# Kernel optimization log

Measured on AMD Instinct MI355X. Metric: run time of the kernel, lower is better.

## Reference

```python
import jax, jax.numpy as jnp
import numpy as np

B, S, E, H = 2, 2048, 1024, 16
HD = E // H


def setup_inputs() -> dict:
    key = jax.random.key(0)
    k1, k2, k3, k4 = jax.random.split(key, 4)
    x = jax.random.normal(k1, (B, S, E), dtype=jnp.float32)
    # nn.Linear(E, 3E, bias=False): weight shape (3E, E), y = x @ W.T
    w_qkv = jax.random.normal(k2, (3 * E, E), dtype=jnp.float32) * (E ** -0.5)
    w_proj = jax.random.normal(k3, (E, E), dtype=jnp.float32) * (E ** -0.5)
    b_proj = jax.random.normal(k4, (E,), dtype=jnp.float32) * 0.02
    return {"x": x, "w_qkv": w_qkv, "w_proj": w_proj, "b_proj": b_proj}


def reference(x, w_qkv, w_proj, b_proj):
    b, s, e = x.shape
    hd = e // H
    qkv = x @ w_qkv.T                                   # (B,S,3E)
    qkv = qkv.reshape(b, s, H, 3, hd)                   # matches view(B,S,H,3*hd).chunk(3,-1)
    q = jnp.transpose(qkv[..., 0, :], (0, 2, 1, 3))      # (B,H,S,hd)
    k = jnp.transpose(qkv[..., 1, :], (0, 2, 1, 3))
    v = jnp.transpose(qkv[..., 2, :], (0, 2, 1, 3))
    scale = hd ** -0.5
    scores = jnp.einsum('bhqd,bhkd->bhqk', q, k) * scale  # (B,H,S,S)
    causal = jnp.tril(jnp.ones((s, s), dtype=bool))
    scores = jnp.where(causal, scores, jnp.float32(-jnp.inf))
    probs = jax.nn.softmax(scores, axis=-1)
    out = jnp.einsum('bhqk,bhkd->bhqd', probs, v)        # (B,H,S,hd)
    out = jnp.transpose(out, (0, 2, 1, 3)).reshape(b, s, e)
    return out @ w_proj.T + b_proj
```

## Files before the change

### kernel.cpp

```cpp
#include <hip/hip_runtime.h>
#include <hip/hip_bf16.h>

#define B_    2
#define S_    2048
#define E_    1024
#define H_    16
#define HD_   64
#define M_    (B_ * S_)
#define QKVN  (3 * E_)

typedef __attribute__((ext_vector_type(8))) short  short8;
typedef __attribute__((ext_vector_type(4))) float  f32x4;

static __device__ __forceinline__ unsigned short f2bf(float f) {
  union { float f; unsigned int u; } c; c.f = f;
  unsigned int u = c.u;
  return (unsigned short)((u + 0x7fffu + ((u >> 16) & 1u)) >> 16);
}

static __device__ __forceinline__ void gload16(unsigned short* lds,
                                               const unsigned short* g) {
  __builtin_amdgcn_global_load_lds(
      (__attribute__((address_space(1))) void*)g,
      (__attribute__((address_space(3))) void*)lds, 16, 0, 0);
}

static __device__ __forceinline__ float dpp_max16(float x) {
  x = fmaxf(x, __int_as_float(__builtin_amdgcn_update_dpp(
          0, __float_as_int(x), 0xB1, 0xF, 0xF, true)));
  x = fmaxf(x, __int_as_float(__builtin_amdgcn_update_dpp(
          0, __float_as_int(x), 0x4E, 0xF, 0xF, true)));
  x = fmaxf(x, __int_as_float(__builtin_amdgcn_update_dpp(
          0, __float_as_int(x), 0x141, 0xF, 0xF, true)));
  x = fmaxf(x, __int_as_float(__builtin_amdgcn_update_dpp(
          0, __float_as_int(x), 0x140, 0xF, 0xF, true)));
  return x;
}
static __device__ __forceinline__ float dpp_sum16(float x) {
  x += __int_as_float(__builtin_amdgcn_update_dpp(
          0, __float_as_int(x), 0xB1, 0xF, 0xF, true));
  x += __int_as_float(__builtin_amdgcn_update_dpp(
          0, __float_as_int(x), 0x4E, 0xF, 0xF, true));
  x += __int_as_float(__builtin_amdgcn_update_dpp(
          0, __float_as_int(x), 0x141, 0xF, 0xF, true));
  x += __int_as_float(__builtin_amdgcn_update_dpp(
          0, __float_as_int(x), 0x140, 0xF, 0xF, true));
  return x;
}

__global__ __launch_bounds__(256) void cvt_f32_to_bf16(
    const float* __restrict__ in, unsigned short* __restrict__ out, int n4) {
  int i = blockIdx.x * 256 + threadIdx.x;
  if (i < n4) {
    float4 v = reinterpret_cast<const float4*>(in)[i];
    ushort4 r;
    r.x = f2bf(v.x); r.y = f2bf(v.y); r.z = f2bf(v.z); r.w = f2bf(v.w);
    reinterpret_cast<ushort4*>(out)[i] = r;
  }
}

template <int BF16_OUT>
__global__ __launch_bounds__(256) void gemm_bt(
    const unsigned short* __restrict__ A, const unsigned short* __restrict__ Bt,
    void* __restrict__ Cout, const float* __restrict__ bias,
    int M, int N, int K, int ldc) {
  __shared__ alignas(16) unsigned short lds_a[128 * 64];
  __shared__ alignas(16) unsigned short lds_b[128 * 64];
  const int t  = threadIdx.x;
  const int w  = t >> 6, l = t & 63, g = l >> 4, lr = l & 15;
  const int bm = blockIdx.y * 128, bn = blockIdx.x * 128;
  const int wr = (w >> 1) * 64,  wc = (w & 1) * 64;

  f32x4 acc[4][4] = {};

  for (int k0 = 0; k0 < K; k0 += 64) {
    __syncthreads();
#pragma unroll
    for (int i = 0; i < 4; i++) {
      const int pass = w * 4 + i;
      const int r = pass * 8 + (l >> 3);
      const int c = (l & 7) ^ (r & 7);
      gload16(lds_a + pass * 512, A + (size_t)(bm + r) * K + k0 + c * 8);
      gload16(lds_b + pass * 512, Bt + (size_t)(bn + r) * K + k0 + c * 8);
    }
    __syncthreads();

    short8 af[4][2], bfr[4][2];
#pragma unroll
    for (int m = 0; m < 4; m++) {
      const int R = wr + m * 16 + lr;
#pragma unroll
      for (int kk = 0; kk < 2; kk++)
        af[m][kk] = *(const short8*)((const char*)lds_a +
            ((R * 128 + kk * 64 + g * 16) ^ ((R & 7) << 4)));
    }
#pragma unroll
    for (int n = 0; n < 4; n++) {
      const int R = wc + n * 16 + lr;
#pragma unroll
      for (int kk = 0; kk < 2; kk++)
        bfr[n][kk] = *(const short8*)((const char*)lds_b +
            ((R * 128 + kk * 64 + g * 16) ^ ((R & 7) << 4)));
    }
#pragma unroll
    for (int m = 0; m < 4; m++)
#pragma unroll
      for (int n = 0; n < 4; n++) {
        acc[m][n] = __builtin_amdgcn_mfma_f32_16x16x32_bf16(
            af[m][0], bfr[n][0], acc[m][n], 0, 0, 0);
        acc[m][n] = __builtin_amdgcn_mfma_f32_16x16x32_bf16(
            af[m][1], bfr[n][1], acc[m][n], 0, 0, 0);
      }
  }

#pragma unroll
  for (int m = 0; m < 4; m++)
#pragma unroll
    for (int n = 0; n < 4; n++)
#pragma unroll
      for (int j = 0; j < 4; j++) {
        const int row = bm + wr + m * 16 + g * 4 + j;
        const int col = bn + wc + n * 16 + lr;
        const float v = acc[m][n][j];
        if constexpr (BF16_OUT) {
          ((unsigned short*)Cout)[(size_t)row * ldc + col] = f2bf(v);
        } else {
          ((float*)Cout)[(size_t)row * ldc + col] = v + bias[col];
        }
      }
}

__global__ __launch_bounds__(256) void attn_fwd(
    const unsigned short* __restrict__ qkv, unsigned short* __restrict__ attn_out) {
  __shared__ alignas(16) unsigned short lds_k[64 * 64];
  __shared__ alignas(16) unsigned short lds_vt[64 * 64];
  __shared__ alignas(16) unsigned short lds_p[4][32 * 64];

  const int t = threadIdx.x;
  const int w = t >> 6, l = t & 63, g = (l >> 4) & 3, lr = l & 15;
  const int bid = blockIdx.x;
  const int bh = bid & 31, b = bh >> 4, h = bh & 15;
  const int rr = bid >> 5;
  const int bx = (rr < 8) ? rr : 23 - rr;
  const int q0 = bx * 128;
  const int qw = q0 + w * 32;
  const unsigned short* base = qkv + (size_t)b * S_ * QKVN + h * (3 * HD_);

  short8 qf[2][2];
#pragma unroll
  for (int m = 0; m < 2; m++) {
    const unsigned short* qp = base + (size_t)(qw + m * 16 + lr) * QKVN + g * 8;
    qf[m][0] = *(const short8*)qp;
    qf[m][1] = *(const short8*)(qp + 32);
  }

  f32x4 o[2][4] = {};
  float m_r[2][4], l_r[2][4];
#pragma unroll
  for (int m = 0; m < 2; m++)
#pragma unroll
    for (int j = 0; j < 4; j++) { m_r[m][j] = -3.0e38f; l_r[m][j] = 0.f; }

  const int numt = 2 * bx + 2;
  const int r_st = t >> 3;
  const int kc   = t & 7;

  short8 kreg[2], vreg[2];
#pragma unroll
  for (int p = 0; p < 2; p++) {
    const unsigned short* kp =
        base + (size_t)(p * 32 + r_st) * QKVN + HD_ + kc * 8;
    kreg[p] = *(const short8*)kp;
    vreg[p] = *(const short8*)(kp + HD_);
  }

  for (int kt = 0; kt < numt; kt++) {
    const int k0 = kt * 64;
#pragma unroll
    for (int p = 0; p < 2; p++) {
      const int r = p * 32 + r_st;
      *(short8*)((char*)lds_k + ((r * 128 + kc * 16) ^ ((r & 7) << 4))) = kreg[p];
#pragma unroll
      for (int j = 0; j < 8; j++) {
        const int d = kc * 8 + j;
        const int swz = ((d & 7) ^ ((d >> 3) & 7)) << 4;
        *(unsigned short*)((char*)lds_vt + ((d * 128 + r * 2) ^ swz)) =
            (unsigned short)vreg[p][j];
      }
    }
    if (kt + 1 < numt) {
#pragma unroll
      for (int p = 0; p < 2; p++) {
        const unsigned short* kp =
            base + (size_t)(k0 + 64 + p * 32 + r_st) * QKVN + HD_ + kc * 8;
        kreg[p] = *(const short8*)kp;
        vreg[p] = *(const short8*)(kp + HD_);
      }
    }
    __syncthreads();

    if (k0 <= qw + 31) {
      f32x4 s[2][4];
      __builtin_amdgcn_s_setprio(1);
#pragma unroll
      for (int n = 0; n < 4; n++) {
        const int R = n * 16 + lr;
        short8 b0 = *(const short8*)((const char*)lds_k +
            ((R * 128 + g * 16) ^ ((R & 7) << 4)));
        short8 b1 = *(const short8*)((const char*)lds_k +
            ((R * 128 + 64 + g * 16) ^ ((R & 7) << 4)));
#pragma unroll
        for (int m = 0; m < 2; m++) {
          f32x4 z = {};
          z = __builtin_amdgcn_mfma_f32_16x16x32_bf16(qf[m][0], b0, z, 0, 0, 0);
          z = __builtin_amdgcn_mfma_f32_16x16x32_bf16(qf[m][1], b1, z, 0, 0, 0);
          s[m][n] = z;
        }
      }
      __builtin_amdgcn_s_setprio(0);

      if (k0 + 63 > qw) {
#pragma unroll
        for (int m = 0; m < 2; m++)
#pragma unroll
          for (int n = 0; n < 4; n++) {
            const int kvc = k0 + n * 16 + lr;
#pragma unroll
            for (int j = 0; j < 4; j++) {
              const int qrow = qw + m * 16 + g * 4 + j;
              if (kvc > qrow) s[m][n][j] = -3.0e38f;
            }
          }
      }

#pragma unroll
      for (int m = 0; m < 2; m++) {
#pragma unroll
        for (int j = 0; j < 4; j++) {
          const float v0 = s[m][0][j] * 0.125f, v1 = s[m][1][j] * 0.125f;
          const float v2 = s[m][2][j] * 0.125f, v3 = s[m][3][j] * 0.125f;
          float mx = dpp_max16(fmaxf(fmaxf(v0, v1), fmaxf(v2, v3)));
          const float mn = fmaxf(m_r[m][j], mx);
          const float c  = __expf(m_r[m][j] - mn);
          m_r[m][j] = mn;
          const float e0 = __expf(v0 - mn), e1 = __expf(v1 - mn);
          const float e2 = __expf(v2 - mn), e3 = __expf(v3 - mn);
          const float sum = dpp_sum16((e0 + e1) + (e2 + e3));
          l_r[m][j] = l_r[m][j] * c + sum;
#pragma unroll
          for (int dt = 0; dt < 4; dt++) o[m][dt][j] *= c;
          const int row = m * 16 + g * 4 + j;
          const int sw  = (row & 7) << 4;
          char* pb = (char*)lds_p[w];
          *(unsigned short*)(pb + ((row * 128 +      lr * 2) ^ sw)) = f2bf(e0);
          *(unsigned short*)(pb + ((row * 128 + 32 + lr * 2) ^ sw)) = f2bf(e1);
          *(unsigned short*)(pb + ((row * 128 + 64 + lr * 2) ^ sw)) = f2bf(e2);
          *(unsigned short*)(pb + ((row * 128 + 96 + lr * 2) ^ sw)) = f2bf(e3);
        }
      }
      __asm__ volatile("s_waitcnt lgkmcnt(0)" ::: "memory");

      __builtin_amdgcn_s_setprio(1);
#pragma unroll
      for (int m = 0; m < 2; m++) {
        const int prow = m * 16 + lr;
        const int psw  = (prow & 7) << 4;
        short8 pf0 = *(const short8*)((const char*)lds_p[w] +
            ((prow * 128 + g * 16) ^ psw));
        short8 pf1 = *(const short8*)((const char*)lds_p[w] +
            ((prow * 128 + 64 + g * 16) ^ psw));
#pragma unroll
        for (int dt = 0; dt < 4; dt++) {
          const int R = dt * 16 + lr;
          const int vsw = ((R & 7) ^ ((R >> 3) & 7)) << 4;
          short8 vf0 = *(const short8*)((const char*)lds_vt +
              ((R * 128 + g * 16) ^ vsw));
          short8 vf1 = *(const short8*)((const char*)lds_vt +
              ((R * 128 + 64 + g * 16) ^ vsw));
          o[m][dt] = __builtin_amdgcn_mfma_f32_16x16x32_bf16(pf0, vf0, o[m][dt], 0, 0, 0);
          o[m][dt] = __builtin_amdgcn_mfma_f32_16x16x32_bf16(pf1, vf1, o[m][dt], 0, 0, 0);
        }
      }
      __builtin_amdgcn_s_setprio(0);
    }

    __syncthreads();
  }

  unsigned short* outp = attn_out + (size_t)b * S_ * E_ + h * HD_;
#pragma unroll
  for (int m = 0; m < 2; m++)
#pragma unroll
    for (int j = 0; j < 4; j++) {
      const float inv = 1.0f / l_r[m][j];
      const int qrow = qw + m * 16 + g * 4 + j;
#pragma unroll
      for (int dt = 0; dt < 4; dt++)
        outp[(size_t)qrow * E_ + dt * 16 + lr] = f2bf(o[m][dt][j] * inv);
    }
}

extern "C" void kernel_launch(void* const* d_in, const int* in_sizes, int n_in,
                              void* d_out, int out_size, void* d_ws, size_t ws_size,
                              hipStream_t stream) {
  (void)in_sizes; (void)n_in; (void)out_size; (void)ws_size;
  const float* x      = (const float*)d_in[0];
  const float* w_qkv  = (const float*)d_in[1];
  const float* w_proj = (const float*)d_in[2];
  const float* b_proj = (const float*)d_in[3];
  float* out = (float*)d_out;

  unsigned short* x_bf     = (unsigned short*)d_ws;
  unsigned short* wqkv_bf  = x_bf    + (size_t)M_ * E_;
  unsigned short* wproj_bf = wqkv_bf + (size_t)QKVN * E_;
  unsigned short* qkv_bf   = wproj_bf + (size_t)E_ * E_;
  unsigned short* attn_bf  = qkv_bf  + (size_t)M_ * QKVN;

  int n4;
  n4 = M_ * E_ / 4;
  cvt_f32_to_bf16<<<(n4 + 255) / 256, 256, 0, stream>>>(x, x_bf, n4);
  n4 = QKVN * E_ / 4;
  cvt_f32_to_bf16<<<(n4 + 255) / 256, 256, 0, stream>>>(w_qkv, wqkv_bf, n4);
  n4 = E_ * E_ / 4;
  cvt_f32_to_bf16<<<(n4 + 255) / 256, 256, 0, stream>>>(w_proj, wproj_bf, n4);

  gemm_bt<1><<<dim3(QKVN / 128, M_ / 128), 256, 0, stream>>>(
      x_bf, wqkv_bf, (void*)qkv_bf, nullptr, M_, QKVN, E_, QKVN);

  attn_fwd<<<dim3(512), 256, 0, stream>>>(qkv_bf, attn_bf);

  gemm_bt<0><<<dim3(E_ / 128, M_ / 128), 256, 0, stream>>>(
      attn_bf, wproj_bf, (void*)out, b_proj, M_, E_, E_, E_);
}
```

Baseline: 226.6 us.

## Transpose attention MFMA operands so each lane owns a query row

Swaps the MFMA operand order in both QK^T and PV so the accumulator holds S^T and O^T, and each lane owns one query row across 16 key columns. Softmax row max and sum then reduce mostly in registers with only two cross-lane shuffles instead of four DPP steps per value. The scale is folded into exp2 via an FMA, P is packed to bf16 with v_cvt_pk_bf16_f32 and written as 8-byte LDS stores, and the output is written as 4-wide vectors. The cost is a new LDS layout for P whose bank-conflict behavior changes, and packed-convert rounding may differ slightly from the old manual bf16 conversion.

Measured after the change: 213.2 us. 1.06x faster.

```diff
diff --git a/kernel.cpp b/kernel.cpp
--- a/kernel.cpp
+++ b/kernel.cpp
@@ -11,6 +11,7 @@
 
 typedef __attribute__((ext_vector_type(8))) short  short8;
 typedef __attribute__((ext_vector_type(4))) float  f32x4;
+typedef __attribute__((ext_vector_type(4))) unsigned short us16x4;
 
 static __device__ __forceinline__ unsigned short f2bf(float f) {
   union { float f; unsigned int u; } c; c.f = f;
@@ -23,29 +24,6 @@
   __builtin_amdgcn_global_load_lds(
       (__attribute__((address_space(1))) void*)g,
       (__attribute__((address_space(3))) void*)lds, 16, 0, 0);
-}
-
-static __device__ __forceinline__ float dpp_max16(float x) {
-  x = fmaxf(x, __int_as_float(__builtin_amdgcn_update_dpp(
-          0, __float_as_int(x), 0xB1, 0xF, 0xF, true)));
-  x = fmaxf(x, __int_as_float(__builtin_amdgcn_update_dpp(
-          0, __float_as_int(x), 0x4E, 0xF, 0xF, true)));
-  x = fmaxf(x, __int_as_float(__builtin_amdgcn_update_dpp(
-          0, __float_as_int(x), 0x141, 0xF, 0xF, true)));
-  x = fmaxf(x, __int_as_float(__builtin_amdgcn_update_dpp(
-          0, __float_as_int(x), 0x140, 0xF, 0xF, true)));
-  return x;
-}
-static __device__ __forceinline__ float dpp_sum16(float x) {
-  x += __int_as_float(__builtin_amdgcn_update_dpp(
-          0, __float_as_int(x), 0xB1, 0xF, 0xF, true));
-  x += __int_as_float(__builtin_amdgcn_update_dpp(
-          0, __float_as_int(x), 0x4E, 0xF, 0xF, true));
-  x += __int_as_float(__builtin_amdgcn_update_dpp(
-          0, __float_as_int(x), 0x141, 0xF, 0xF, true));
-  x += __int_as_float(__builtin_amdgcn_update_dpp(
-          0, __float_as_int(x), 0x140, 0xF, 0xF, true));
-  return x;
 }
 
 __global__ __launch_bounds__(256) void cvt_f32_to_bf16(
@@ -155,11 +133,9 @@
   }
 
   f32x4 o[2][4] = {};
-  float m_r[2][4], l_r[2][4];
-#pragma unroll
-  for (int m = 0; m < 2; m++)
-#pragma unroll
-    for (int j = 0; j < 4; j++) { m_r[m][j] = -3.0e38f; l_r[m][j] = 0.f; }
+  float m_r[2] = {-3.0e38f, -3.0e38f};
+  float l_r[2] = {0.f, 0.f};
+  const float SCALE2 = 0.18033688011112042f;
 
   const int numt = 2 * bx + 2;
   const int r_st = t >> 3;
@@ -200,85 +176,103 @@
     __syncthreads();
 
     if (k0 <= qw + 31) {
-      f32x4 s[2][4];
+      f32x4 st[2][4];
       __builtin_amdgcn_s_setprio(1);
 #pragma unroll
       for (int n = 0; n < 4; n++) {
         const int R = n * 16 + lr;
-        short8 b0 = *(const short8*)((const char*)lds_k +
-            ((R * 128 + g * 16) ^ ((R & 7) << 4)));
-        short8 b1 = *(const short8*)((const char*)lds_k +
-            ((R * 128 + 64 + g * 16) ^ ((R & 7) << 4)));
+        const int sw = (R & 7) << 4;
+        short8 kf0 = *(const short8*)((const char*)lds_k +
+            ((R * 128 + g * 16) ^ sw));
+        short8 kf1 = *(const short8*)((const char*)lds_k +
+            ((R * 128 + 64 + g * 16) ^ sw));
 #pragma unroll
         for (int m = 0; m < 2; m++) {
           f32x4 z = {};
-          z = __builtin_amdgcn_mfma_f32_16x16x32_bf16(qf[m][0], b0, z, 0, 0, 0);
-          z = __builtin_amdgcn_mfma_f32_16x16x32_bf16(qf[m][1], b1, z, 0, 0, 0);
-          s[m][n] = z;
+          z = __builtin_amdgcn_mfma_f32_16x16x32_bf16(kf0, qf[m][0], z, 0, 0, 0);
+          z = __builtin_amdgcn_mfma_f32_16x16x32_bf16(kf1, qf[m][1], z, 0, 0, 0);
+          st[m][n] = z;
         }
       }
       __builtin_amdgcn_s_setprio(0);
 
-      if (k0 + 63 > qw) {
-#pragma unroll
-        for (int m = 0; m < 2; m++)
-#pragma unroll
-          for (int n = 0; n < 4; n++) {
-            const int kvc = k0 + n * 16 + lr;
-#pragma unroll
-            for (int j = 0; j < 4; j++) {
-              const int qrow = qw + m * 16 + g * 4 + j;
-              if (kvc > qrow) s[m][n][j] = -3.0e38f;
-            }
+      const bool diag = (k0 + 63 > qw);
+
+#pragma unroll
+      for (int m = 0; m < 2; m++) {
+        const int qrow = qw + m * 16 + lr;
+        if (diag) {
+#pragma unroll
+          for (int n = 0; n < 4; n++)
+#pragma unroll
+            for (int j = 0; j < 4; j++)
+              if ((k0 + n * 16 + g * 4 + j) > qrow) st[m][n][j] = -3.0e38f;
+        }
+        float mx = st[m][0][0];
+#pragma unroll
+        for (int n = 0; n < 4; n++)
+#pragma unroll
+          for (int j = 0; j < 4; j++) mx = fmaxf(mx, st[m][n][j]);
+        mx = fmaxf(mx, __shfl_xor(mx, 16, 64));
+        mx = fmaxf(mx, __shfl_xor(mx, 32, 64));
+        const float mn = fmaxf(m_r[m], mx * SCALE2);
+        const float c  = exp2f(m_r[m] - mn);
+        m_r[m] = mn;
+        float p[4][4];
+        float sum = 0.f;
+#pragma unroll
+        for (int n = 0; n < 4; n++)
+#pragma unroll
+          for (int j = 0; j < 4; j++) {
+            p[n][j] = exp2f(fmaf(st[m][n][j], SCALE2, -mn));
+            sum += p[n][j];
           }
-      }
-
+        sum += __shfl_xor(sum, 16, 64);
+        sum += __shfl_xor(sum, 32, 64);
+        l_r[m] = l_r[m] * c + sum;
+#pragma unroll
+        for (int dt = 0; dt < 4; dt++) o[m][dt] *= c;
+        char* pb = (char*)lds_p[w];
+        const int rowb = (m * 16 + lr) * 128;
+        const int sw   = (lr & 7) << 4;
+#pragma unroll
+        for (int n = 0; n < 4; n++) {
+          unsigned w0, w1;
+          __asm__("v_cvt_pk_bf16_f32 %0, %1, %2"
+                  : "=v"(w0) : "v"(p[n][0]), "v"(p[n][1]));
+          __asm__("v_cvt_pk_bf16_f32 %0, %1, %2"
+                  : "=v"(w1) : "v"(p[n][2]), "v"(p[n][3]));
+          uint2 val; val.x = w0; val.y = w1;
+          *(uint2*)(pb + ((rowb + n * 32 + g * 8) ^ sw)) = val;
+        }
+      }
+      __asm__ volatile("s_waitcnt lgkmcnt(0)" ::: "memory");
+
+      short8 pf[2][2];
 #pragma unroll
       for (int m = 0; m < 2; m++) {
-#pragma unroll
-        for (int j = 0; j < 4; j++) {
-          const float v0 = s[m][0][j] * 0.125f, v1 = s[m][1][j] * 0.125f;
-          const float v2 = s[m][2][j] * 0.125f, v3 = s[m][3][j] * 0.125f;
-          float mx = dpp_max16(fmaxf(fmaxf(v0, v1), fmaxf(v2, v3)));
-          const float mn = fmaxf(m_r[m][j], mx);
-          const float c  = __expf(m_r[m][j] - mn);
-          m_r[m][j] = mn;
-          const float e0 = __expf(v0 - mn), e1 = __expf(v1 - mn);
-          const float e2 = __expf(v2 - mn), e3 = __expf(v3 - mn);
-          const float sum = dpp_sum16((e0 + e1) + (e2 + e3));
-          l_r[m][j] = l_r[m][j] * c + sum;
-#pragma unroll
-          for (int dt = 0; dt < 4; dt++) o[m][dt][j] *= c;
-          const int row = m * 16 + g * 4 + j;
-          const int sw  = (row & 7) << 4;
-          char* pb = (char*)lds_p[w];
-          *(unsigned short*)(pb + ((row * 128 +      lr * 2) ^ sw)) = f2bf(e0);
-          *(unsigned short*)(pb + ((row * 128 + 32 + lr * 2) ^ sw)) = f2bf(e1);
-          *(unsigned short*)(pb + ((row * 128 + 64 + lr * 2) ^ sw)) = f2bf(e2);
-          *(unsigned short*)(pb + ((row * 128 + 96 + lr * 2) ^ sw)) = f2bf(e3);
-        }
-      }
-      __asm__ volatile("s_waitcnt lgkmcnt(0)" ::: "memory");
-
+        const int rowb = (m * 16 + lr) * 128;
+        const int sw   = (lr & 7) << 4;
+        pf[m][0] = *(const short8*)((const char*)lds_p[w] +
+            ((rowb + g * 16) ^ sw));
+        pf[m][1] = *(const short8*)((const char*)lds_p[w] +
+            ((rowb + 64 + g * 16) ^ sw));
+      }
       __builtin_amdgcn_s_setprio(1);
 #pragma unroll
-      for (int m = 0; m < 2; m++) {
-        const int prow = m * 16 + lr;
-        const int psw  = (prow & 7) << 4;
-        short8 pf0 = *(const short8*)((const char*)lds_p[w] +
-            ((prow * 128 + g * 16) ^ psw));
-        short8 pf1 = *(const short8*)((const char*)lds_p[w] +
-            ((prow * 128 + 64 + g * 16) ^ psw));
-#pragma unroll
-        for (int dt = 0; dt < 4; dt++) {
-          const int R = dt * 16 + lr;
-          const int vsw = ((R & 7) ^ ((R >> 3) & 7)) << 4;
-          short8 vf0 = *(const short8*)((const char*)lds_vt +
-              ((R * 128 + g * 16) ^ vsw));
-          short8 vf1 = *(const short8*)((const char*)lds_vt +
-              ((R * 128 + 64 + g * 16) ^ vsw));
-          o[m][dt] = __builtin_amdgcn_mfma_f32_16x16x32_bf16(pf0, vf0, o[m][dt], 0, 0, 0);
-          o[m][dt] = __builtin_amdgcn_mfma_f32_16x16x32_bf16(pf1, vf1, o[m][dt], 0, 0, 0);
+      for (int dt = 0; dt < 4; dt++) {
+        const int R = dt * 16 + lr;
+        const int vsw = ((R & 7) ^ ((R >> 3) & 7)) << 4;
+        short8 vf0 = *(const short8*)((const char*)lds_vt +
+            ((R * 128 + g * 16) ^ vsw));
+        short8 vf1 = *(const short8*)((const char*)lds_vt +
+            ((R * 128 + 64 + g * 16) ^ vsw));
+#pragma unroll
+        for (int m = 0; m < 2; m++) {
+          o[m][dt] = __builtin_amdgcn_mfma_f32_16x16x32_bf16(
+              vf0, pf[m][0], o[m][dt], 0, 0, 0);
+          o[m][dt] = __builtin_amdgcn_mfma_f32_16x16x32_bf16(
+              vf1, pf[m][1], o[m][dt], 0, 0, 0);
         }
       }
       __builtin_amdgcn_s_setprio(0);
@@ -289,15 +283,17 @@
 
   unsigned short* outp = attn_out + (size_t)b * S_ * E_ + h * HD_;
 #pragma unroll
-  for (int m = 0; m < 2; m++)
-#pragma unroll
-    for (int j = 0; j < 4; j++) {
-      const float inv = 1.0f / l_r[m][j];
-      const int qrow = qw + m * 16 + g * 4 + j;
-#pragma unroll
-      for (int dt = 0; dt < 4; dt++)
-        outp[(size_t)qrow * E_ + dt * 16 + lr] = f2bf(o[m][dt][j] * inv);
-    }
+  for (int m = 0; m < 2; m++) {
+    const float inv = 1.0f / l_r[m];
+    const int qrow = qw + m * 16 + lr;
+#pragma unroll
+    for (int dt = 0; dt < 4; dt++) {
+      us16x4 w4;
+#pragma unroll
+      for (int j = 0; j < 4; j++) w4[j] = f2bf(o[m][dt][j] * inv);
+      *(us16x4*)(outp + (size_t)qrow * E_ + dt * 16 + g * 4) = w4;
+    }
+  }
 }
 
 extern "C" void kernel_launch(void* const* d_in, const int* in_sizes, int n_in,
```
